# Kernel optimization log

Hardware: AMD Instinct MI355X
Metric: run time of the kernel (lower is better)

## Reference

```python
import jax, jax.numpy as jnp
import numpy as np

HIDDEN = 512
OUTDIM = 256
D = (HIDDEN + 1) * (HIDDEN + 1)
EPS = 1e-5


def setup_inputs() -> dict:
    key = jax.random.key(0)
    k1, k2, k3, k4 = jax.random.split(key, 4)
    B = 128
    a = jax.random.normal(k1, (B, HIDDEN), dtype=jnp.float32)
    v = jax.random.normal(k2, (B, HIDDEN), dtype=jnp.float32)
    # learned params
    ln_gamma = jnp.ones((D,), dtype=jnp.float32)
    ln_beta = jnp.zeros((D,), dtype=jnp.float32)
    W = jax.random.normal(k3, (OUTDIM, D), dtype=jnp.float32) / np.sqrt(D)
    b = jax.random.normal(k4, (OUTDIM,), dtype=jnp.float32) * 0.01
    return {"a": a, "v": v, "ln_gamma": ln_gamma, "ln_beta": ln_beta, "W": W, "b": b}


def reference(a, v, ln_gamma, ln_beta, W, b):
    B = a.shape[0]
    ones = jnp.ones((B, 1), dtype=a.dtype)
    ah = jnp.concatenate([ones, a], axis=1)  # [B, H+1]
    vh = jnp.concatenate([ones, v], axis=1)  # [B, H+1]
    # rank-1 outer product, flattened: [B, (H+1)^2]
    fusion = jnp.einsum('bi,bj->bij', ah, vh).reshape(B, D)
    # LayerNorm over last dim
    mu = jnp.mean(fusion, axis=-1, keepdims=True)
    var = jnp.mean(jnp.square(fusion - mu), axis=-1, keepdims=True)
    normed = (fusion - mu) / jnp.sqrt(var + EPS) * ln_gamma + ln_beta
    # dropout = identity (eval mode)
    out = jax.nn.relu(normed @ W.T + b)
    return out
```

## Files before the change

### kernel.cpp

```cpp
#include <hip/hip_runtime.h>
#include <hip/hip_bf16.h>

#define HID 512
#define OD  256
#define HP  513
#define EPSV 1e-5f

typedef float f32x16 __attribute__((ext_vector_type(16)));
typedef short s16x8  __attribute__((ext_vector_type(8)));

static __device__ __forceinline__ unsigned short f2bf(float f) {
    union { float f; unsigned u; } x; x.f = f;
    unsigned r = x.u + 0x7FFFu + ((x.u >> 16) & 1u);
    return (unsigned short)(r >> 16);
}
static __device__ __forceinline__ unsigned pkbf(float x, float y) {
    float2 t; t.x = x; t.y = y;
    __hip_bfloat162 h = __float22bfloat162_rn(t);
    union { __hip_bfloat162 h; unsigned u; } c; c.h = h;
    return c.u;
}
static __device__ __forceinline__ float bfu(unsigned short u) {
    union { unsigned q; float f; } cv; cv.q = ((unsigned)u) << 16;
    return cv.f;
}


__global__ void prep_all(const float* __restrict__ a, const float* __restrict__ v,
                         const float* __restrict__ gamma, const float* __restrict__ beta,
                         unsigned short* __restrict__ gpb, unsigned short* __restrict__ bpb,
                         unsigned short* __restrict__ vhT, float* __restrict__ vh512,
                         float* __restrict__ ahT, float* __restrict__ mu,
                         float* __restrict__ rsig) {
    __shared__ float s1[256], s2[256], s3[256], s4[256];
    int b = blockIdx.x, t = threadIdx.x;
    if (b < HP) {
        int ii = b;
        for (int s = t; s < 512; s += 256) {
            int half = s >> 8, ss = s & 255, ll = ss >> 3, c = ss & 7;
            int j = half * 256 + c * 32 + ll;
            gpb[(size_t)ii * 512 + s] = f2bf(gamma[(size_t)ii * HP + j]);
            bpb[(size_t)ii * 512 + s] = f2bf(beta [(size_t)ii * HP + j]);
        }
    } else if (b < HP + 128) {
        int m = b - HP;
        for (int s = t; s < 512; s += 256) {
            int half = s >> 8, ss = s & 255, ll = ss >> 3, c = ss & 7;
            int j = half * 256 + c * 32 + ll;
            float val = (j == 0) ? 1.f : v[m * HID + j - 1];
            vhT[(size_t)m * 512 + s] = f2bf(val);
        }
    } else if (b == HP + 128) {
        if (t < 128) vh512[t] = v[t * HID + 511];
    } else if (b < HP + 129 + 257) {
        int idx = (b - HP - 129) * 256 + t;
        if (idx < HP * 128) {
            int i = idx >> 7, m = idx & 127;
            ahT[idx] = (i == 0) ? 1.f : a[m * HID + i - 1];
        }
    } else {
        int m = b - (HP + 129 + 257);
        float a0 = a[m * HID + t], a1 = a[m * HID + t + 256];
        float v0 = v[m * HID + t], v1 = v[m * HID + t + 256];
        s1[t] = a0 + a1; s2[t] = a0 * a0 + a1 * a1;
        s3[t] = v0 + v1; s4[t] = v0 * v0 + v1 * v1;
        __syncthreads();
        for (int off = 128; off > 0; off >>= 1) {
            if (t < off) { s1[t] += s1[t + off]; s2[t] += s2[t + off];
                           s3[t] += s3[t + off]; s4[t] += s4[t + off]; }
            __syncthreads();
        }
        if (t == 0) {
            float Sa = 1.f + s1[0], Qa = 1.f + s2[0];
            float Sv = 1.f + s3[0], Qv = 1.f + s4[0];
            float muv = Sa * Sv / (float)((float)HP * (float)HP);
            float var = Qa * Qv / (float)((float)HP * (float)HP) - muv * muv;
            mu[m]   = muv;
            rsig[m] = rsqrtf(var + EPSV);
        }
    }
}

__global__ __launch_bounds__(512, 2) void stage_fused(
        const float* __restrict__ W, const unsigned short* __restrict__ gpb,
        const unsigned short* __restrict__ bpb, const unsigned short* __restrict__ vhT,
        const float* __restrict__ ahT, const float* __restrict__ gamma,
        const float* __restrict__ beta, float* __restrict__ w5g, float* __restrict__ w5b,
        float* __restrict__ Pout, float* __restrict__ Sgo, float* __restrict__ Sbo) {
    __shared__ __align__(16) char Bs[131072];
    __shared__ __align__(16) char bt[2][16384];

    const int tid = threadIdx.x, lane = tid & 63, w = tid >> 6;
    const int l31 = lane & 31, kg = lane >> 5;
    const int cr = 2 * w + kg;
    const int colm = (w & 3) * 32 + l31;
    const int kslb = (w >> 2) * 8;
    const int o = blockIdx.x;
    const unsigned rbase = (unsigned)o * 513u;

    float w5w0 = W[(size_t)(rbase + (unsigned)tid) * 513u + 512u];
    float g50  = gamma[(size_t)tid * 513u + 512u];
    float b50  = beta [(size_t)tid * 513u + 512u];
    float w5w1 = 0.f, g51 = 0.f, b51 = 0.f;
    if (tid == 0) {
        w5w1 = W[(size_t)(rbase + 512u) * 513u + 512u];
        g51  = gamma[(size_t)512 * 513u + 512u];
        b51  = beta [(size_t)512 * 513u + 512u];
    }

#pragma unroll
    for (int q0 = 0; q0 < 16; q0 += 4) {
        uint4 vals[4];
#pragma unroll
        for (int qq = 0; qq < 4; ++qq) {
            int idx = tid + (q0 + qq) * 512;
            int mr = idx >> 6, c = idx & 63;
            vals[qq] = *(const uint4*)(vhT + (size_t)mr * 512 + c * 8);
        }
#pragma unroll
        for (int qq = 0; qq < 4; ++qq) {
            int idx = tid + (q0 + qq) * 512;
            int mr = idx >> 6, c = idx & 63;
            *(uint4*)(&Bs[mr * 1024 + ((c * 16) ^ ((mr & 15) << 4))]) = vals[qq];
        }
    }

    w5g[(size_t)o * HP + tid] = g50 * w5w0;
    w5b[(size_t)o * HP + tid] = b50 * w5w0;
    if (tid == 0) {
        w5g[(size_t)o * HP + 512] = g51 * w5w1;
        w5b[(size_t)o * HP + 512] = b51 * w5w1;
    }

    float WrA[16], WrB[16];
    uint4 gaA1, gaA2, gaB1, gaB2;
    float ahv[16];
    f32x16 acc;
#pragma unroll
    for (int e = 0; e < 16; ++e) acc[e] = 0.f;
    float psum = 0.f, sg = 0.f, sb = 0.f;

    auto LOADW = [&](int g, int half, float (&dst)[16]) {
        const float* p1 = W + (size_t)(rbase + (unsigned)(g * 32 + cr)) * 513u + half * 256 + l31;
        const float* p2 = p1 + 16 * 513;
#pragma unroll
        for (int c = 0; c < 8; ++c) { dst[c] = p1[c * 32]; dst[8 + c] = p2[c * 32]; }
    };
    auto LOADG = [&](int g, int half, uint4& u1, uint4& u2) {
        u1 = *(const uint4*)(gpb + ((size_t)(g * 32 + cr) << 9) + half * 256 + l31 * 8);
        u2 = *(const uint4*)(gpb + ((size_t)(g * 32 + cr + 16) << 9) + half * 256 + l31 * 8);
    };
    auto CONVROW = [&](const float* Wc, const uint4 gc, const uint4 b4, int row, char* tile) {
        const unsigned gw[4] = {gc.x, gc.y, gc.z, gc.w};
        const unsigned bw[4] = {b4.x, b4.y, b4.z, b4.w};
        float p[8];
        float s = 0.f, t2 = 0.f;
#pragma unroll
        for (int e = 0; e < 8; ++e) {
            unsigned ug = (e & 1) ? (gw[e >> 1] >> 16) : (gw[e >> 1] & 0xffffu);
            unsigned ub = (e & 1) ? (bw[e >> 1] >> 16) : (bw[e >> 1] & 0xffffu);
            p[e] = bfu((unsigned short)ug) * Wc[e];
            s += p[e];
            t2 = fmaf(bfu((unsigned short)ub), Wc[e], t2);
        }
        uint4 o4;
        o4.x = pkbf(p[0], p[1]); o4.y = pkbf(p[2], p[3]);
        o4.z = pkbf(p[4], p[5]); o4.w = pkbf(p[6], p[7]);
        *(uint4*)(tile + row * 512 + ((l31 * 16) ^ ((row & 15) << 4))) = o4;
        sg += s; sb += t2;
    };

    LOADW(0, 0, WrA); LOADG(0, 0, gaA1, gaA2);
    __syncthreads();

#pragma unroll 1
    for (int g = 0; g < 16; ++g) {
        uint4 bb1 = *(const uint4*)(bpb + ((size_t)(g * 32 + cr) << 9) + l31 * 8);
        uint4 bb2 = *(const uint4*)(bpb + ((size_t)(g * 32 + cr + 16) << 9) + l31 * 8);
        LOADW(g, 1, WrB); LOADG(g, 1, gaB1, gaB2);
        CONVROW(&WrA[0], gaA1, bb1, cr,      bt[0]);
        CONVROW(&WrA[8], gaA2, bb2, cr + 16, bt[0]);

        __builtin_amdgcn_sched_barrier(0);
        asm volatile("s_waitcnt lgkmcnt(0)" ::: "memory");
        __builtin_amdgcn_s_barrier();
        __builtin_amdgcn_sched_barrier(0);

#pragma unroll
        for (int i2 = 0; i2 < 8; ++i2) {
            int ksl = kslb + i2;
            s16x8 afr = *(const s16x8*)(&bt[0][l31 * 512 +
                          ((ksl * 32 + kg * 16) ^ ((l31 & 15) << 4))]);
            s16x8 bfr = *(const s16x8*)(&Bs[colm * 1024 +
                          ((ksl * 32 + kg * 16) ^ ((colm & 15) << 4))]);
            acc = __builtin_amdgcn_mfma_f32_32x32x16_bf16(afr, bfr, acc, 0, 0, 0);
        }

        uint4 cb1 = *(const uint4*)(bpb + ((size_t)(g * 32 + cr) << 9) + 256 + l31 * 8);
        uint4 cb2 = *(const uint4*)(bpb + ((size_t)(g * 32 + cr + 16) << 9) + 256 + l31 * 8);
        if (g < 15) { LOADW(g + 1, 0, WrA); LOADG(g + 1, 0, gaA1, gaA2); }
#pragma unroll
        for (int e = 0; e < 16; ++e) {
            int row32 = (e & 3) + 8 * (e >> 2) + 4 * kg;
            ahv[e] = ahT[(size_t)(g * 32 + row32) * 128 + colm];
        }
        CONVROW(&WrB[0], gaB1, cb1, cr,      bt[1]);
        CONVROW(&WrB[8], gaB2, cb2, cr + 16, bt[1]);

        __builtin_amdgcn_sched_barrier(0);
        asm volatile("s_waitcnt lgkmcnt(0)" ::: "memory");
        __builtin_amdgcn_s_barrier();
        __builtin_amdgcn_sched_barrier(0);

#pragma unroll
        for (int i2 = 0; i2 < 8; ++i2) {
            int ksl = kslb + i2;
            s16x8 afr = *(const s16x8*)(&bt[1][l31 * 512 +
                          ((ksl * 32 + kg * 16) ^ ((l31 & 15) << 4))]);
            s16x8 bfr = *(const s16x8*)(&Bs[colm * 1024 +
                          ((512 + ksl * 32 + kg * 16) ^ ((colm & 15) << 4))]);
            acc = __builtin_amdgcn_mfma_f32_32x32x16_bf16(afr, bfr, acc, 0, 0, 0);
        }
#pragma unroll
        for (int e = 0; e < 16; ++e) psum = fmaf(acc[e], ahv[e], psum);
#pragma unroll
        for (int e = 0; e < 16; ++e) acc[e] = 0.f;
    }

    __syncthreads();
    float* redP  = (float*)Bs;
    float* redSg = redP + 256;
    float* redSb = redP + 264;
    psum += __shfl_xor(psum, 32);
#pragma unroll
    for (int off = 1; off < 64; off <<= 1) {
        sg += __shfl_xor(sg, off); sb += __shfl_xor(sb, off);
    }
    if (lane < 32) redP[colm * 2 + (w >> 2)] = psum;
    if (lane == 0) { redSg[w] = sg; redSb[w] = sb; }
    __syncthreads();
    if (tid < 128) Pout[(size_t)o * 128 + tid] = redP[tid * 2] + redP[tid * 2 + 1];
    if (tid == 0) {
        float S = 0.f, T = 0.f;
#pragma unroll
        for (int k = 0; k < 8; ++k) { S += redSg[k]; T += redSb[k]; }
        Sgo[o] = S; Sbo[o] = T;
    }
}

__global__ void finalize_kernel(const float* __restrict__ Pout, const float* __restrict__ Sgo,
                                const float* __restrict__ Sbo, const float* __restrict__ w5g,
                                const float* __restrict__ w5b, const float* __restrict__ ahT,
                                const float* __restrict__ vh512, const unsigned short* __restrict__ vhT,
                                const float* __restrict__ W, const float* __restrict__ gamma,
                                const float* __restrict__ beta, const float* __restrict__ mu,
                                const float* __restrict__ rsig, const float* __restrict__ bias,
                                float* __restrict__ out) {
    __shared__ float wg[HP], wb[HP], gws[512], bws[512];
    int o = blockIdx.x, m = threadIdx.x;
    for (int i = m; i < HP; i += 128) {
        wg[i] = w5g[(size_t)o * HP + i];
        wb[i] = w5b[(size_t)o * HP + i];
    }
    for (int j = m; j < 512; j += 128) {
        float wv = W[((size_t)o * 513u + 512u) * 513u + j];
        int s = ((j >> 8) << 8) + ((j & 31) << 3) + ((j & 255) >> 5);
        gws[s] = gamma[(size_t)512 * HP + j] * wv;
        bws[s] = beta [(size_t)512 * HP + j] * wv;
    }
    __syncthreads();
    float Pf = 0.f, Sgf = 0.f, Sbf = 0.f;
    for (int i = 0; i < HP; ++i) {
        float g = wg[i];
        Pf = fmaf(ahT[(size_t)i * 128 + m], g, Pf);
        Sgf += g; Sbf += wb[i];
    }
    float dot = 0.f, Sg2 = 0.f, Sb2 = 0.f;
    const unsigned short* vr = vhT + (size_t)m * 512;
    for (int s = 0; s < 512; ++s) {
        float g = gws[s];
        dot = fmaf(bfu(vr[s]), g, dot);
        Sg2 += g; Sb2 += bws[s];
    }
    float P  = Pout[(size_t)o * 128 + m] + vh512[m] * Pf + ahT[(size_t)512 * 128 + m] * dot;
    float Sg = Sgo[o] + Sgf + Sg2;
    float Sb = Sbo[o] + Sbf + Sb2;
    float x = rsig[m] * (P - mu[m] * Sg) + Sb + bias[o];
    out[m * OD + o] = fmaxf(x, 0.f);
}

extern "C" void kernel_launch(void* const* d_in, const int* in_sizes, int n_in,
                              void* d_out, int out_size, void* d_ws, size_t ws_size,
                              hipStream_t stream) {
    const float* a     = (const float*)d_in[0];
    const float* v     = (const float*)d_in[1];
    const float* gamma = (const float*)d_in[2];
    const float* beta  = (const float*)d_in[3];
    const float* W     = (const float*)d_in[4];
    const float* bias  = (const float*)d_in[5];
    float* out = (float*)d_out;

    float* cur = (float*)d_ws;
    float* mu    = cur; cur += 128;
    float* rsig  = cur; cur += 128;
    float* Sgo   = cur; cur += 256;
    float* Sbo   = cur; cur += 256;
    float* Pout  = cur; cur += (size_t)OD * 128;
    float* ahT   = cur; cur += (size_t)HP * 128;
    float* vh512 = cur; cur += 128;
    float* w5g   = cur; cur += (size_t)OD * HP;
    float* w5b   = cur; cur += (size_t)OD * HP;
    unsigned short* gpb = (unsigned short*)cur;
    unsigned short* bpb = gpb + (size_t)HP * 512;
    unsigned short* vhT = bpb + (size_t)HP * 512;

    prep_all<<<HP + 129 + 257 + 128, 256, 0, stream>>>(a, v, gamma, beta, gpb, bpb,
                                                       vhT, vh512, ahT, mu, rsig);
    stage_fused<<<OD, 512, 0, stream>>>(W, gpb, bpb, vhT, ahT, gamma, beta, w5g, w5b,
                                        Pout, Sgo, Sbo);
    finalize_kernel<<<OD, 128, 0, stream>>>(Pout, Sgo, Sbo, w5g, w5b, ahT, vh512, vhT,
                                            W, gamma, beta, mu, rsig, bias, out);
}
```

Measured before the change: 99.42 us.

## Fuse finalize kernel into stage_fused epilogue using shared-memory reductions

Removes the separate finalize kernel and performs its per-output-column reductions (Pf, dot, gamma/beta sums) inside the tail of stage_fused, split across 4 thread groups of 128 and combined via LDS. This drops a kernel launch and the Pout/Sgo/Sbo round trip through global memory. The vhT row is read from the already-resident Bs tile, and the scratch buffers reuse the bt region. It relies on w5g/w5b for block o being written earlier in the same kernel by that same block, and it lengthens the tail of each block.

```diff
diff --git a/kernel.cpp b/kernel.cpp
--- a/kernel.cpp
+++ b/kernel.cpp
@@ -86,7 +86,9 @@
         const unsigned short* __restrict__ bpb, const unsigned short* __restrict__ vhT,
         const float* __restrict__ ahT, const float* __restrict__ gamma,
         const float* __restrict__ beta, float* __restrict__ w5g, float* __restrict__ w5b,
-        float* __restrict__ Pout, float* __restrict__ Sgo, float* __restrict__ Sbo) {
+        const float* __restrict__ vh512, const float* __restrict__ mu,
+        const float* __restrict__ rsig, const float* __restrict__ bias,
+        float* __restrict__ out) {
     __shared__ __align__(16) char Bs[131072];
     __shared__ __align__(16) char bt[2][16384];
 
@@ -228,9 +230,19 @@
     }
 
     __syncthreads();
-    float* redP  = (float*)Bs;
+    float* redP  = (float*)bt;
     float* redSg = redP + 256;
     float* redSb = redP + 264;
+    float* bcST  = redP + 272;
+    float* wgL   = redP + 288;
+    float* wbL   = wgL + 520;
+    float* gwsL  = wbL + 520;
+    float* bwsL  = gwsL + 512;
+    float* PfP   = bwsL + 512;
+    float* dotP  = PfP + 512;
+    float* sgP   = dotP + 512;
+    float* sbP   = sgP + 4;
+
     psum += __shfl_xor(psum, 32);
 #pragma unroll
     for (int off = 1; off < 64; off <<= 1) {
@@ -238,55 +250,58 @@
     }
     if (lane < 32) redP[colm * 2 + (w >> 2)] = psum;
     if (lane == 0) { redSg[w] = sg; redSb[w] = sb; }
+    {
+        wgL[tid] = w5g[(size_t)o * HP + tid];
+        wbL[tid] = w5b[(size_t)o * HP + tid];
+        if (tid == 0) {
+            wgL[512] = w5g[(size_t)o * HP + 512];
+            wbL[512] = w5b[(size_t)o * HP + 512];
+        }
+        float wv = W[(size_t)(rbase + 512u) * 513u + (unsigned)tid];
+        int s = ((tid >> 8) << 8) + ((tid & 31) << 3) + ((tid & 255) >> 5);
+        gwsL[s] = gamma[(size_t)512 * HP + tid] * wv;
+        bwsL[s] = beta [(size_t)512 * HP + tid] * wv;
+    }
     __syncthreads();
-    if (tid < 128) Pout[(size_t)o * 128 + tid] = redP[tid * 2] + redP[tid * 2 + 1];
     if (tid == 0) {
         float S = 0.f, T = 0.f;
 #pragma unroll
         for (int k = 0; k < 8; ++k) { S += redSg[k]; T += redSb[k]; }
-        Sgo[o] = S; Sbo[o] = T;
-    }
-}
-
-__global__ void finalize_kernel(const float* __restrict__ Pout, const float* __restrict__ Sgo,
-                                const float* __restrict__ Sbo, const float* __restrict__ w5g,
-                                const float* __restrict__ w5b, const float* __restrict__ ahT,
-                                const float* __restrict__ vh512, const unsigned short* __restrict__ vhT,
-                                const float* __restrict__ W, const float* __restrict__ gamma,
-                                const float* __restrict__ beta, const float* __restrict__ mu,
-                                const float* __restrict__ rsig, const float* __restrict__ bias,
-                                float* __restrict__ out) {
-    __shared__ float wg[HP], wb[HP], gws[512], bws[512];
-    int o = blockIdx.x, m = threadIdx.x;
-    for (int i = m; i < HP; i += 128) {
-        wg[i] = w5g[(size_t)o * HP + i];
-        wb[i] = w5b[(size_t)o * HP + i];
-    }
-    for (int j = m; j < 512; j += 128) {
-        float wv = W[((size_t)o * 513u + 512u) * 513u + j];
-        int s = ((j >> 8) << 8) + ((j & 31) << 3) + ((j & 255) >> 5);
-        gws[s] = gamma[(size_t)512 * HP + j] * wv;
-        bws[s] = beta [(size_t)512 * HP + j] * wv;
+        bcST[0] = S; bcST[1] = T;
+    }
+    {
+        const int h = tid >> 7, m2 = tid & 127;
+        float Pf = 0.f, dt = 0.f, sgf = 0.f, sbf = 0.f;
+        for (int i = h; i < 513; i += 4) {
+            float g = wgL[i];
+            Pf = fmaf(ahT[(size_t)i * 128 + m2], g, Pf);
+            sgf += g; sbf += wbL[i];
+        }
+        for (int c = h; c < 64; c += 4) {
+            s16x8 vv = *(const s16x8*)(&Bs[m2 * 1024 + ((c * 16) ^ ((m2 & 15) << 4))]);
+            const float* gp  = gwsL + c * 8;
+            const float* bp2 = bwsL + c * 8;
+#pragma unroll
+            for (int e = 0; e < 8; ++e) {
+                dt = fmaf(bfu((unsigned short)vv[e]), gp[e], dt);
+                sgf += gp[e]; sbf += bp2[e];
+            }
+        }
+        PfP[h * 128 + m2] = Pf; dotP[h * 128 + m2] = dt;
+        if (m2 == 0) { sgP[h] = sgf; sbP[h] = sbf; }
     }
     __syncthreads();
-    float Pf = 0.f, Sgf = 0.f, Sbf = 0.f;
-    for (int i = 0; i < HP; ++i) {
-        float g = wg[i];
-        Pf = fmaf(ahT[(size_t)i * 128 + m], g, Pf);
-        Sgf += g; Sbf += wb[i];
-    }
-    float dot = 0.f, Sg2 = 0.f, Sb2 = 0.f;
-    const unsigned short* vr = vhT + (size_t)m * 512;
-    for (int s = 0; s < 512; ++s) {
-        float g = gws[s];
-        dot = fmaf(bfu(vr[s]), g, dot);
-        Sg2 += g; Sb2 += bws[s];
-    }
-    float P  = Pout[(size_t)o * 128 + m] + vh512[m] * Pf + ahT[(size_t)512 * 128 + m] * dot;
-    float Sg = Sgo[o] + Sgf + Sg2;
-    float Sb = Sbo[o] + Sbf + Sb2;
-    float x = rsig[m] * (P - mu[m] * Sg) + Sb + bias[o];
-    out[m * OD + o] = fmaxf(x, 0.f);
+    if (tid < 128) {
+        int m = tid;
+        float Pb  = redP[m * 2] + redP[m * 2 + 1];
+        float Pft = PfP[m] + PfP[128 + m] + PfP[256 + m] + PfP[384 + m];
+        float dtt = dotP[m] + dotP[128 + m] + dotP[256 + m] + dotP[384 + m];
+        float Sg  = bcST[0] + sgP[0] + sgP[1] + sgP[2] + sgP[3];
+        float Sb  = bcST[1] + sbP[0] + sbP[1] + sbP[2] + sbP[3];
+        float P   = Pb + vh512[m] * Pft + ahT[(size_t)512 * 128 + m] * dtt;
+        float x   = rsig[m] * (P - mu[m] * Sg) + Sb + bias[o];
+        out[m * OD + o] = fmaxf(x, 0.f);
+    }
 }
 
 extern "C" void kernel_launch(void* const* d_in, const int* in_sizes, int n_in,
@@ -303,9 +318,6 @@
     float* cur = (float*)d_ws;
     float* mu    = cur; cur += 128;
     float* rsig  = cur; cur += 128;
-    float* Sgo   = cur; cur += 256;
-    float* Sbo   = cur; cur += 256;
-    float* Pout  = cur; cur += (size_t)OD * 128;
     float* ahT   = cur; cur += (size_t)HP * 128;
     float* vh512 = cur; cur += 128;
     float* w5g   = cur; cur += (size_t)OD * HP;
@@ -317,7 +329,5 @@
     prep_all<<<HP + 129 + 257 + 128, 256, 0, stream>>>(a, v, gamma, beta, gpb, bpb,
                                                        vhT, vh512, ahT, mu, rsig);
     stage_fused<<<OD, 512, 0, stream>>>(W, gpb, bpb, vhT, ahT, gamma, beta, w5g, w5b,
-                                        Pout, Sgo, Sbo);
-    finalize_kernel<<<OD, 128, 0, stream>>>(Pout, Sgo, Sbo, w5g, w5b, ahT, vh512, vhT,
-                                            W, gamma, beta, mu, rsig, bias, out);
-}
+                                        vh512, mu, rsig, bias, out);
+}
```

Measured after the change: 87.34 us. 12.2% less time.
